# Optimization experiments

Hardware: AMD Instinct MI355X
Metric: run time of the kernel (lower is better)

## Reference

```python
import jax, jax.numpy as jnp
import numpy as np


def setup_inputs() -> dict:
    key = jax.random.key(0)
    k1, k2 = jax.random.split(key)
    B, C, H, W = 16, 128, 32, 32   # C == embedding_dim
    K = 2048                        # codebook size (num_embeddings)
    x = jax.random.normal(k1, (B, C, H, W), dtype=jnp.float32)
    codebook = jax.random.normal(k2, (K, C), dtype=jnp.float32)
    return {"x": x, "codebook": codebook}


def reference(x, codebook):
    # x: [B, C, H, W] -> NHWC -> flatten to [N, C]
    B, C, H, W = x.shape
    x_nhwc = jnp.transpose(x, (0, 2, 3, 1))
    x_flat = x_nhwc.reshape(-1, C)                      # [N, C]
    # Squared L2 distances via expansion (argmin-equivalent to torch.norm
    # of the broadcast difference, without the [N, K, C] intermediate):
    x_sq = jnp.sum(x_flat * x_flat, axis=1, keepdims=True)   # [N, 1]
    w_sq = jnp.sum(codebook * codebook, axis=1)              # [K]
    d2 = x_sq - 2.0 * (x_flat @ codebook.T) + w_sq           # [N, K]
    encoding_indices = jnp.argmin(d2, axis=1)                # [N]
    encodings = jax.nn.one_hot(encoding_indices, codebook.shape[0],
                               dtype=x_flat.dtype)           # [N, K]
    quantized = encodings @ codebook                         # [N, C]
    quantized = jnp.transpose(quantized.reshape(B, H, W, C), (0, 3, 1, 2))
    return encodings, quantized
```

## Files before the change

### kernel.cpp

```cpp
#include <hip/hip_runtime.h>
#include <hip/hip_bf16.h>

#define N_TOK  16384
#define KCODES 2048
#define CDIM   128
#define BM     64
#define TPB    512
#define NCW    8
#define CPW    (KCODES / NCW)
#define TPW    (CPW / 16)
#define CAP    40
#define DELTA  5.0f
#define ASTR   68
#define FILLB  2048

typedef __attribute__((ext_vector_type(8))) short bhalf8;
typedef __attribute__((ext_vector_type(4))) float facc4;

__global__ __launch_bounds__(256) void fillprep_kernel(const float* __restrict__ cb,
                                                       bhalf8* __restrict__ cbt,
                                                       float* __restrict__ wsq,
                                                       float4* __restrict__ enc4) {
    if (blockIdx.x < KCODES / 16) {
        const int T   = blockIdx.x;
        const int tid = threadIdx.x;
        const int r   = tid >> 4;
        const int g   = tid & 15;
        const float4* src = (const float4*)(cb + ((size_t)(T * 16 + r)) * CDIM + g * 8);
        float4 a0 = src[0], a1 = src[1];

        float s = a0.x*a0.x + a0.y*a0.y + a0.z*a0.z + a0.w*a0.w
                + a1.x*a1.x + a1.y*a1.y + a1.z*a1.z + a1.w*a1.w;
        s += __shfl_xor(s, 1, 64);
        s += __shfl_xor(s, 2, 64);
        s += __shfl_xor(s, 4, 64);
        s += __shfl_xor(s, 8, 64);
        if (g == 0) wsq[T * 16 + r] = s;

        union { unsigned u[4]; bhalf8 v; } fu;
        __hip_bfloat162 h0 = __float22bfloat162_rn(make_float2(a0.x, a0.y));
        __hip_bfloat162 h1 = __float22bfloat162_rn(make_float2(a0.z, a0.w));
        __hip_bfloat162 h2 = __float22bfloat162_rn(make_float2(a1.x, a1.y));
        __hip_bfloat162 h3 = __float22bfloat162_rn(make_float2(a1.z, a1.w));
        fu.u[0] = *(unsigned*)&h0; fu.u[1] = *(unsigned*)&h1;
        fu.u[2] = *(unsigned*)&h2; fu.u[3] = *(unsigned*)&h3;
        const int kf = g >> 2, q = g & 3;
        cbt[(size_t)T * 256 + kf * 64 + q * 16 + r] = fu.v;
    }

    const float4 z4 = {0.f, 0.f, 0.f, 0.f};
    const size_t total = (size_t)N_TOK * KCODES / 4;
    size_t i = (size_t)blockIdx.x * 256 + threadIdx.x;
    #pragma unroll 4
    for (; i < total; i += (size_t)FILLB * 256) enc4[i] = z4;
}

__global__ __launch_bounds__(TPB, 1) void argmin_kernel(const float* __restrict__ x,
                                                        const float* __restrict__ cb,
                                                        const bhalf8* __restrict__ cbt,
                                                        const float* __restrict__ wsqg,
                                                        float* __restrict__ enc,
                                                        float* __restrict__ quant) {
    __shared__ float As[CDIM][ASTR];
    __shared__ float wsqs[KCODES];
    __shared__ float redvw[NCW][BM];
    __shared__ float rowthr[BM];
    __shared__ int   cnt[BM];
    __shared__ int   candk[BM][CAP];
    __shared__ int   rowidx[BM];

    const int tid  = threadIdx.x;
    const int lane = tid & 63;
    const int w    = tid >> 6;
    const int q    = lane >> 4;
    const int r    = lane & 15;
    const int n0   = blockIdx.x * BM;
    const int b    = n0 >> 10;
    const int hw0  = n0 & 1023;

    {
        int m4 = (tid & 15) << 2;
        int c0 = tid >> 4;
        #pragma unroll
        for (int i = 0; i < 4; i++) {
            int c = c0 + 32 * i;
            float4 v = *(const float4*)(x + (((size_t)(b * CDIM + c)) << 10) + hw0 + m4);
            *(float4*)(&As[c][m4]) = v;
        }
    }
    #pragma unroll
    for (int i = 0; i < KCODES / TPB; i++) wsqs[i * TPB + tid] = wsqg[i * TPB + tid];
    if (tid < BM) cnt[tid] = 0;
    __syncthreads();

    bhalf8 af[4][4];
    #pragma unroll
    for (int rt = 0; rt < 4; rt++) {
        int m = rt * 16 + r;
        #pragma unroll
        for (int kf = 0; kf < 4; kf++) {
            union { unsigned u[4]; bhalf8 v; } fu;
            #pragma unroll
            for (int p = 0; p < 4; p++) {
                int k = kf * 32 + q * 8 + 2 * p;
                __hip_bfloat162 h = __float22bfloat162_rn(make_float2(As[k][m], As[k + 1][m]));
                fu.u[p] = *(unsigned*)&h;
            }
            af[rt][kf] = fu.v;
        }
    }

    const int    cw  = w * CPW;
    const size_t tb0 = (size_t)(cw >> 4) * 256;

    {
        float rmin[16];
        #pragma unroll
        for (int t = 0; t < 16; t++) rmin[t] = 3.0e38f;

        bhalf8 bcur[4], bnxt[4];
        #pragma unroll
        for (int kf = 0; kf < 4; kf++) bcur[kf] = cbt[tb0 + kf * 64 + lane];
        #pragma unroll
        for (int kf = 0; kf < 4; kf++) bnxt[kf] = cbt[tb0 + 256 + kf * 64 + lane];

        for (int t = 0; t < TPW; t++) {
            bhalf8 bn2[4];
            if (t + 2 < TPW) {
                size_t tb = tb0 + (size_t)(t + 2) * 256;
                #pragma unroll
                for (int kf = 0; kf < 4; kf++) bn2[kf] = cbt[tb + kf * 64 + lane];
            }
            facc4 acc[4];
            #pragma unroll
            for (int rt = 0; rt < 4; rt++) acc[rt] = (facc4){0.f, 0.f, 0.f, 0.f};
            #pragma unroll
            for (int kf = 0; kf < 4; kf++)
                #pragma unroll
                for (int rt = 0; rt < 4; rt++)
                    acc[rt] = __builtin_amdgcn_mfma_f32_16x16x32_bf16(af[rt][kf], bcur[kf], acc[rt], 0, 0, 0);
            float wv = wsqs[cw + t * 16 + r];
            #pragma unroll
            for (int rt = 0; rt < 4; rt++)
                #pragma unroll
                for (int i = 0; i < 4; i++)
                    rmin[rt * 4 + i] = fminf(rmin[rt * 4 + i], fmaf(-2.f, acc[rt][i], wv));
            #pragma unroll
            for (int kf = 0; kf < 4; kf++) { bcur[kf] = bnxt[kf]; bnxt[kf] = bn2[kf]; }
        }
        #pragma unroll
        for (int t = 0; t < 16; t++) {
            float v = rmin[t];
            v = fminf(v, __shfl_xor(v, 1, 64));
            v = fminf(v, __shfl_xor(v, 2, 64));
            v = fminf(v, __shfl_xor(v, 4, 64));
            v = fminf(v, __shfl_xor(v, 8, 64));
            if (r == 0) redvw[w][(t >> 2) * 16 + q * 4 + (t & 3)] = v;
        }
    }
    __syncthreads();
    if (tid < BM) {
        float mv = redvw[0][tid];
        #pragma unroll
        for (int j = 1; j < NCW; j++) mv = fminf(mv, redvw[j][tid]);
        rowthr[tid] = mv + DELTA;
    }
    __syncthreads();

    {
        float thr[16];
        #pragma unroll
        for (int t = 0; t < 16; t++) thr[t] = rowthr[(t >> 2) * 16 + q * 4 + (t & 3)];

        bhalf8 bcur[4], bnxt[4];
        #pragma unroll
        for (int kf = 0; kf < 4; kf++) bcur[kf] = cbt[tb0 + kf * 64 + lane];
        #pragma unroll
        for (int kf = 0; kf < 4; kf++) bnxt[kf] = cbt[tb0 + 256 + kf * 64 + lane];

        for (int t = 0; t < TPW; t++) {
            bhalf8 bn2[4];
            if (t + 2 < TPW) {
                size_t tb = tb0 + (size_t)(t + 2) * 256;
                #pragma unroll
                for (int kf = 0; kf < 4; kf++) bn2[kf] = cbt[tb + kf * 64 + lane];
            }
            facc4 acc[4];
            #pragma unroll
            for (int rt = 0; rt < 4; rt++) acc[rt] = (facc4){0.f, 0.f, 0.f, 0.f};
            #pragma unroll
            for (int kf = 0; kf < 4; kf++)
                #pragma unroll
                for (int rt = 0; rt < 4; rt++)
                    acc[rt] = __builtin_amdgcn_mfma_f32_16x16x32_bf16(af[rt][kf], bcur[kf], acc[rt], 0, 0, 0);
            float wv = wsqs[cw + t * 16 + r];
            #pragma unroll
            for (int rt = 0; rt < 4; rt++)
                #pragma unroll
                for (int i = 0; i < 4; i++) {
                    float d = fmaf(-2.f, acc[rt][i], wv);
                    if (d <= thr[rt * 4 + i]) {
                        int row = rt * 16 + q * 4 + i;
                        int p = atomicAdd(&cnt[row], 1);
                        if (p < CAP) candk[row][p] = cw + t * 16 + r;
                    }
                }
            #pragma unroll
            for (int kf = 0; kf < 4; kf++) { bcur[kf] = bnxt[kf]; bnxt[kf] = bn2[kf]; }
        }
    }
    __syncthreads();

    for (int m = 8 * w; m < 8 * w + 8; m++) {
        int c = min(cnt[m], CAP);
        float bv = 3.0e38f; int bk = 0x7fffffff;
        for (int t = 0; t < c; t++) {
            int k = candk[m][t];
            float x0 = As[lane][m], x1 = As[lane + 64][m];
            float c0 = cb[(size_t)k * CDIM + lane];
            float c1 = cb[(size_t)k * CDIM + 64 + lane];
            float s = x0 * c0 + x1 * c1;
            #pragma unroll
            for (int off = 1; off <= 32; off <<= 1) s += __shfl_xor(s, off, 64);
            float d = fmaf(-2.f, s, wsqs[k]);
            if (d < bv || (d == bv && k < bk)) { bv = d; bk = k; }
        }
        if (lane == 0) rowidx[m] = bk;
    }
    __syncthreads();

    if (tid < BM) enc[(size_t)(n0 + tid) * KCODES + rowidx[tid]] = 1.0f;

    #pragma unroll
    for (int i = tid; i < BM * CDIM / 4; i += TPB) {
        int c  = i >> 4;
        int hq = (i & 15) << 2;
        float4 v;
        v.x = cb[(size_t)rowidx[hq + 0] * CDIM + c];
        v.y = cb[(size_t)rowidx[hq + 1] * CDIM + c];
        v.z = cb[(size_t)rowidx[hq + 2] * CDIM + c];
        v.w = cb[(size_t)rowidx[hq + 3] * CDIM + c];
        *(float4*)(quant + (((size_t)(b * CDIM + c)) << 10) + hw0 + hq) = v;
    }
}

extern "C" void kernel_launch(void* const* d_in, const int* in_sizes, int n_in,
                              void* d_out, int out_size, void* d_ws, size_t ws_size,
                              hipStream_t stream) {
    const float* x  = (const float*)d_in[0];
    const float* cb = (const float*)d_in[1];
    float* out = (float*)d_out;

    bhalf8* cbt  = (bhalf8*)d_ws;
    float*  wsqp = (float*)((char*)d_ws + 512 * 1024);

    fillprep_kernel<<<FILLB, 256, 0, stream>>>(cb, cbt, wsqp, (float4*)out);
    argmin_kernel<<<N_TOK / BM, TPB, 0, stream>>>(x, cb, cbt, wsqp,
                                                  out, out + (size_t)N_TOK * KCODES);
}
```

Measured before the change: 223.8 us.

## Split argmin waves into 2x4 row/code groups and restructure encoding zero-fill

Each of the 8 waves now handles 2 of the 4 row tiles over a quarter of the codebook, where before every wave took all 4 row tiles over an eighth of it. This halves each wave's A-fragment and accumulator register footprint but doubles the codebook fragment loads per MFMA, so B-operand traffic grows in exchange for lower register pressure. The zero-fill of the encodings buffer also changes from a grid-stride loop to a fixed contiguous 4096-float4 chunk per block, issued before the codebook prep.

```diff
diff --git a/kernel.cpp b/kernel.cpp
--- a/kernel.cpp
+++ b/kernel.cpp
@@ -6,8 +6,9 @@
 #define CDIM   128
 #define BM     64
 #define TPB    512
-#define NCW    8
-#define CPW    (KCODES / NCW)
+#define NRG    2
+#define NCG    4
+#define CPW    (KCODES / NCG)
 #define TPW    (CPW / 16)
 #define CAP    40
 #define DELTA  5.0f
@@ -21,6 +22,13 @@
                                                        bhalf8* __restrict__ cbt,
                                                        float* __restrict__ wsq,
                                                        float4* __restrict__ enc4) {
+    {
+        const float4 z4 = {0.f, 0.f, 0.f, 0.f};
+        float4* dst = enc4 + (size_t)blockIdx.x * 4096;
+        #pragma unroll
+        for (int j = 0; j < 16; j++) dst[j * 256 + threadIdx.x] = z4;
+    }
+
     if (blockIdx.x < KCODES / 16) {
         const int T   = blockIdx.x;
         const int tid = threadIdx.x;
@@ -47,12 +55,6 @@
         const int kf = g >> 2, q = g & 3;
         cbt[(size_t)T * 256 + kf * 64 + q * 16 + r] = fu.v;
     }
-
-    const float4 z4 = {0.f, 0.f, 0.f, 0.f};
-    const size_t total = (size_t)N_TOK * KCODES / 4;
-    size_t i = (size_t)blockIdx.x * 256 + threadIdx.x;
-    #pragma unroll 4
-    for (; i < total; i += (size_t)FILLB * 256) enc4[i] = z4;
 }
 
 __global__ __launch_bounds__(TPB, 1) void argmin_kernel(const float* __restrict__ x,
@@ -63,7 +65,7 @@
                                                         float* __restrict__ quant) {
     __shared__ float As[CDIM][ASTR];
     __shared__ float wsqs[KCODES];
-    __shared__ float redvw[NCW][BM];
+    __shared__ float redvw[NCG][BM];
     __shared__ float rowthr[BM];
     __shared__ int   cnt[BM];
     __shared__ int   candk[BM][CAP];
@@ -74,6 +76,8 @@
     const int w    = tid >> 6;
     const int q    = lane >> 4;
     const int r    = lane & 15;
+    const int rg   = w & 1;
+    const int cg   = w >> 1;
     const int n0   = blockIdx.x * BM;
     const int b    = n0 >> 10;
     const int hw0  = n0 & 1023;
@@ -93,10 +97,10 @@
     if (tid < BM) cnt[tid] = 0;
     __syncthreads();
 
-    bhalf8 af[4][4];
+    bhalf8 af[2][4];
     #pragma unroll
-    for (int rt = 0; rt < 4; rt++) {
-        int m = rt * 16 + r;
+    for (int rt = 0; rt < 2; rt++) {
+        int m = (rg * 2 + rt) * 16 + r;
         #pragma unroll
         for (int kf = 0; kf < 4; kf++) {
             union { unsigned u[4]; bhalf8 v; } fu;
@@ -110,13 +114,13 @@
         }
     }
 
-    const int    cw  = w * CPW;
+    const int    cw  = cg * CPW;
     const size_t tb0 = (size_t)(cw >> 4) * 256;
 
     {
-        float rmin[16];
-        #pragma unroll
-        for (int t = 0; t < 16; t++) rmin[t] = 3.0e38f;
+        float rmin[8];
+        #pragma unroll
+        for (int t = 0; t < 8; t++) rmin[t] = 3.0e38f;
 
         bhalf8 bcur[4], bnxt[4];
         #pragma unroll
@@ -131,17 +135,17 @@
                 #pragma unroll
                 for (int kf = 0; kf < 4; kf++) bn2[kf] = cbt[tb + kf * 64 + lane];
             }
-            facc4 acc[4];
-            #pragma unroll
-            for (int rt = 0; rt < 4; rt++) acc[rt] = (facc4){0.f, 0.f, 0.f, 0.f};
+            facc4 acc[2];
+            #pragma unroll
+            for (int rt = 0; rt < 2; rt++) acc[rt] = (facc4){0.f, 0.f, 0.f, 0.f};
             #pragma unroll
             for (int kf = 0; kf < 4; kf++)
                 #pragma unroll
-                for (int rt = 0; rt < 4; rt++)
+                for (int rt = 0; rt < 2; rt++)
                     acc[rt] = __builtin_amdgcn_mfma_f32_16x16x32_bf16(af[rt][kf], bcur[kf], acc[rt], 0, 0, 0);
             float wv = wsqs[cw + t * 16 + r];
             #pragma unroll
-            for (int rt = 0; rt < 4; rt++)
+            for (int rt = 0; rt < 2; rt++)
                 #pragma unroll
                 for (int i = 0; i < 4; i++)
                     rmin[rt * 4 + i] = fminf(rmin[rt * 4 + i], fmaf(-2.f, acc[rt][i], wv));
@@ -149,28 +153,27 @@
             for (int kf = 0; kf < 4; kf++) { bcur[kf] = bnxt[kf]; bnxt[kf] = bn2[kf]; }
         }
         #pragma unroll
-        for (int t = 0; t < 16; t++) {
+        for (int t = 0; t < 8; t++) {
             float v = rmin[t];
             v = fminf(v, __shfl_xor(v, 1, 64));
             v = fminf(v, __shfl_xor(v, 2, 64));
             v = fminf(v, __shfl_xor(v, 4, 64));
             v = fminf(v, __shfl_xor(v, 8, 64));
-            if (r == 0) redvw[w][(t >> 2) * 16 + q * 4 + (t & 3)] = v;
+            if (r == 0) redvw[cg][(rg * 2 + (t >> 2)) * 16 + q * 4 + (t & 3)] = v;
         }
     }
     __syncthreads();
     if (tid < BM) {
-        float mv = redvw[0][tid];
-        #pragma unroll
-        for (int j = 1; j < NCW; j++) mv = fminf(mv, redvw[j][tid]);
+        float mv = fminf(fminf(redvw[0][tid], redvw[1][tid]),
+                         fminf(redvw[2][tid], redvw[3][tid]));
         rowthr[tid] = mv + DELTA;
     }
     __syncthreads();
 
     {
-        float thr[16];
-        #pragma unroll
-        for (int t = 0; t < 16; t++) thr[t] = rowthr[(t >> 2) * 16 + q * 4 + (t & 3)];
+        float thr[8];
+        #pragma unroll
+        for (int t = 0; t < 8; t++) thr[t] = rowthr[(rg * 2 + (t >> 2)) * 16 + q * 4 + (t & 3)];
 
         bhalf8 bcur[4], bnxt[4];
         #pragma unroll
@@ -185,22 +188,22 @@
                 #pragma unroll
                 for (int kf = 0; kf < 4; kf++) bn2[kf] = cbt[tb + kf * 64 + lane];
             }
-            facc4 acc[4];
-            #pragma unroll
-            for (int rt = 0; rt < 4; rt++) acc[rt] = (facc4){0.f, 0.f, 0.f, 0.f};
+            facc4 acc[2];
+            #pragma unroll
+            for (int rt = 0; rt < 2; rt++) acc[rt] = (facc4){0.f, 0.f, 0.f, 0.f};
             #pragma unroll
             for (int kf = 0; kf < 4; kf++)
                 #pragma unroll
-                for (int rt = 0; rt < 4; rt++)
+                for (int rt = 0; rt < 2; rt++)
                     acc[rt] = __builtin_amdgcn_mfma_f32_16x16x32_bf16(af[rt][kf], bcur[kf], acc[rt], 0, 0, 0);
             float wv = wsqs[cw + t * 16 + r];
             #pragma unroll
-            for (int rt = 0; rt < 4; rt++)
+            for (int rt = 0; rt < 2; rt++)
                 #pragma unroll
                 for (int i = 0; i < 4; i++) {
                     float d = fmaf(-2.f, acc[rt][i], wv);
                     if (d <= thr[rt * 4 + i]) {
-                        int row = rt * 16 + q * 4 + i;
+                        int row = (rg * 2 + rt) * 16 + q * 4 + i;
                         int p = atomicAdd(&cnt[row], 1);
                         if (p < CAP) candk[row][p] = cw + t * 16 + r;
                     }
```

Result: slower. 234.6 us (+4.8%).
